# Optimization experiments

Measured on AMD Instinct MI355X. Metric: run time of the kernel, lower is better.

The kernel has to match this reference:

```python
import jax, jax.numpy as jnp
import numpy as np

K = 20  # neighbors

def _graph_feature(x, k):
    # x: (B, N, 3) -> (B, 3, N, k) neighbor features (DGCNN-style gather)
    inner = -2.0 * jnp.einsum('bnd,bmd->bnm', x, x)
    xx = jnp.sum(x * x, axis=2, keepdims=True)              # (B, N, 1)
    pairwise = -xx - inner - jnp.swapaxes(xx, 1, 2)          # (B, N, N) = -||xi-xj||^2
    _, idx = jax.lax.top_k(pairwise, k)                      # (B, N, k) nearest neighbors
    feat = jax.vmap(lambda xb, ib: xb[ib])(x, idx)           # (B, N, k, 3)
    return jnp.transpose(feat, (0, 3, 1, 2))                 # (B, 3, N, k)

def _vn_layer(x, w, scale, shift):
    # matmul over channel dim, folded-BN affine, relu
    y = jnp.einsum('oc,bcnk->bonk', w, x)
    y = y * scale[None, :, None, None] + shift[None, :, None, None]
    return jax.nn.relu(y)

def setup_inputs() -> dict:
    key = jax.random.key(0)
    ks = jax.random.split(key, 12)
    B, N = 32, 256
    inp = {
        'x': jax.random.normal(ks[0], (B, N, 3), dtype=jnp.float32),
        'w1': jax.random.normal(ks[1], (64, 3), dtype=jnp.float32),
        's1': jnp.ones((64,), jnp.float32), 't1': jnp.zeros((64,), jnp.float32),
        'w2': jax.random.normal(ks[2], (128, 64), dtype=jnp.float32) * 0.1,
        's2': jnp.ones((128,), jnp.float32), 't2': jnp.zeros((128,), jnp.float32),
        'w3': jax.random.normal(ks[3], (256, 128), dtype=jnp.float32) * 0.1,
        's3': jnp.ones((256,), jnp.float32), 't3': jnp.zeros((256,), jnp.float32),
        'fc1_w': jax.random.normal(ks[4], (128, 256), dtype=jnp.float32) * 0.05,
        'fc1_b': jnp.zeros((128,), jnp.float32),
        'fc2_w': jax.random.normal(ks[5], (40, 128), dtype=jnp.float32) * 0.05,
        'fc2_b': jnp.zeros((40,), jnp.float32),
    }
    return inp

def reference(x, w1, s1, t1, w2, s2, t2, w3, s3, t3, fc1_w, fc1_b, fc2_w, fc2_b):
    h = _graph_feature(x, K)                                 # (B, 3, N, k)
    h = jax.nn.relu(_vn_layer(h, w1, s1, t1))                # double relu as in source
    h = jax.nn.relu(_vn_layer(h, w2, s2, t2))
    h = jax.nn.relu(_vn_layer(h, w3, s3, t3))                # (B, 256, N, k)
    h = jnp.max(h, axis=-1)                                  # (B, 256, N) with N==256
    h = jax.nn.relu(h @ fc1_w.T + fc1_b)                     # Linear over last axis
    return h @ fc2_w.T + fc2_b                               # (B, 256, 40)
```

## Files before the change

kernel.cpp:

```cpp
#include <hip/hip_runtime.h>
#include <hip/hip_bf16.h>

#define B_ 32
#define N_ 256
#define K_ 20
#define C1 64
#define C2 128
#define C3 256
#define F1 128
#define F2 40
#define NEG_INF (-3.402823466e38f)

__global__ __launch_bounds__(256) void k_front(const float* __restrict__ x,
    const float* __restrict__ w1, const float* __restrict__ s1, const float* __restrict__ b1,
    const float* __restrict__ w2, const float* __restrict__ s2, const float* __restrict__ b2,
    const float* __restrict__ w3, const float* __restrict__ s3, const float* __restrict__ b3,
    const float* __restrict__ fc1w,
    int* __restrict__ idx, float* __restrict__ P, float* __restrict__ fc1T) {

    __shared__ float smem[3136];
    const int blk  = blockIdx.x;
    const int t    = threadIdx.x;
    const int lane = t & 63;
    const int wv   = t >> 6;

    if (blk < 512) {
        float* xs = smem;
        float* y1 = smem + 64;
        float* y2 = smem + 1088;
        const int pbase = blk * 16;
        const int og = t >> 2;
        const int p0 = (t & 3) * 4;

        if (t < 48) xs[t] = x[(size_t)pbase * 3 + t];
        __syncthreads();

        {
            const int oc = lane;
            const float wa = w1[oc * 3 + 0], wb = w1[oc * 3 + 1], wc = w1[oc * 3 + 2];
            const float sc = s1[oc], sh = b1[oc];
            const int q0 = wv * 4;
            float4 v;
            #pragma unroll
            for (int p = 0; p < 4; ++p) {
                const int pp = q0 + p;
                float vv = wa * xs[pp * 3 + 0] + wb * xs[pp * 3 + 1] + wc * xs[pp * 3 + 2];
                (&v.x)[p] = fmaxf(vv * sc + sh, 0.0f);
            }
            *(float4*)&y1[oc * 16 + q0] = v;
        }
        __syncthreads();

        {
            const int oc0 = og * 2;
            float acc[2][4] = {};
            for (int k = 0; k < C1; k += 4) {
                float4 a[4];
                #pragma unroll
                for (int kk = 0; kk < 4; ++kk)
                    a[kk] = *(const float4*)&y1[(k + kk) * 16 + p0];
                const float4 wA = *(const float4*)(w2 + (size_t)oc0 * C1 + k);
                const float4 wB = *(const float4*)(w2 + (size_t)(oc0 + 1) * C1 + k);
                #pragma unroll
                for (int kk = 0; kk < 4; ++kk) {
                    #pragma unroll
                    for (int p = 0; p < 4; ++p) {
                        acc[0][p] += (&wA.x)[kk] * (&a[kk].x)[p];
                        acc[1][p] += (&wB.x)[kk] * (&a[kk].x)[p];
                    }
                }
            }
            const float sc0 = s2[oc0], sh0 = b2[oc0];
            const float sc1 = s2[oc0 + 1], sh1 = b2[oc0 + 1];
            float4 v0, v1;
            #pragma unroll
            for (int p = 0; p < 4; ++p) {
                (&v0.x)[p] = fmaxf(acc[0][p] * sc0 + sh0, 0.0f);
                (&v1.x)[p] = fmaxf(acc[1][p] * sc1 + sh1, 0.0f);
            }
            *(float4*)&y2[oc0 * 16 + p0]       = v0;
            *(float4*)&y2[(oc0 + 1) * 16 + p0] = v1;
        }
        __syncthreads();

        {
            const int oc0 = og * 4;
            float acc[4][4] = {};
            for (int k = 0; k < C2; k += 4) {
                float4 a[4];
                #pragma unroll
                for (int kk = 0; kk < 4; ++kk)
                    a[kk] = *(const float4*)&y2[(k + kk) * 16 + p0];
                float4 w[4];
                #pragma unroll
                for (int o = 0; o < 4; ++o)
                    w[o] = *(const float4*)(w3 + (size_t)(oc0 + o) * C2 + k);
                #pragma unroll
                for (int o = 0; o < 4; ++o) {
                    #pragma unroll
                    for (int kk = 0; kk < 4; ++kk) {
                        const float wvv = (&w[o].x)[kk];
                        #pragma unroll
                        for (int p = 0; p < 4; ++p)
                            acc[o][p] += wvv * (&a[kk].x)[p];
                    }
                }
            }
            const float4 sc = *(const float4*)&s3[oc0];
            const float4 sh = *(const float4*)&b3[oc0];
            #pragma unroll
            for (int p = 0; p < 4; ++p) {
                float4 v;
                #pragma unroll
                for (int o = 0; o < 4; ++o)
                    (&v.x)[o] = fmaxf(acc[o][p] * (&sc.x)[o] + (&sh.x)[o], 0.0f);
                *(float4*)&P[(size_t)(pbase + p0 + p) * C3 + oc0] = v;
            }
        }

    } else if (blk < 2560) {
        const int tb = blk - 512;
        const int b  = tb >> 6;
        const int n  = ((tb & 63) << 2) | wv;
        const int bn = (b << 8) | n;
        const float* xb = x + (size_t)b * N_ * 3;

        const float nx = xb[n * 3 + 0], ny = xb[n * 3 + 1], nz = xb[n * 3 + 2];
        const float xxn = nx * nx + ny * ny + nz * nz;

        unsigned k0, k1, k2, k3;
        {
            unsigned kk[4];
            #pragma unroll
            for (int i = 0; i < 4; ++i) {
                const int m = lane + (i << 6);
                const float cx = xb[m * 3 + 0], cy = xb[m * 3 + 1], cz = xb[m * 3 + 2];
                const float xxm = cx * cx + cy * cy + cz * cz;
                const float v = 2.0f * (nx * cx + ny * cy + nz * cz) - xxn - xxm;
                const unsigned u = __float_as_uint(v);
                kk[i] = (u & 0x80000000u) ? ~u : (u | 0x80000000u);
            }
            k0 = kk[0]; k1 = kk[1]; k2 = kk[2]; k3 = kk[3];
        }

        unsigned prefix = 0u;
        #pragma unroll
        for (int bit = 30; bit >= 0; --bit) {
            const unsigned cand = prefix | (1u << bit);
            const int c = __popcll(__ballot(k0 >= cand))
                        + __popcll(__ballot(k1 >= cand))
                        + __popcll(__ballot(k2 >= cand))
                        + __popcll(__ballot(k3 >= cand));
            if (c >= K_) prefix = cand;
        }
        const unsigned T = prefix;

        int* op = idx + (size_t)bn * K_;
        const unsigned long long lt = (1ull << lane) - 1ull;

        const unsigned long long G0 = __ballot(k0 > T);
        const unsigned long long G1 = __ballot(k1 > T);
        const unsigned long long G2 = __ballot(k2 > T);
        const unsigned long long G3 = __ballot(k3 > T);
        const int n0 = __popcll(G0), n1 = __popcll(G1), n2 = __popcll(G2), n3 = __popcll(G3);
        const int g = n0 + n1 + n2 + n3;
        if (k0 > T) op[          __popcll(G0 & lt)] = lane;
        if (k1 > T) op[n0      + __popcll(G1 & lt)] = 64  | lane;
        if (k2 > T) op[n0 + n1 + __popcll(G2 & lt)] = 128 | lane;
        if (k3 > T) op[n0 + n1 + n2 + __popcll(G3 & lt)] = 192 | lane;

        const int e = K_ - g;
        const unsigned long long E0 = __ballot(k0 == T);
        const unsigned long long E1 = __ballot(k1 == T);
        const unsigned long long E2 = __ballot(k2 == T);
        const unsigned long long E3 = __ballot(k3 == T);
        const int m0 = __popcll(E0), m1 = __popcll(E1), m2 = __popcll(E2);
        if (k0 == T) { const int p = __popcll(E0 & lt);                 if (p < e) op[g + p] = lane; }
        if (k1 == T) { const int p = m0 + __popcll(E1 & lt);            if (p < e) op[g + p] = 64  | lane; }
        if (k2 == T) { const int p = m0 + m1 + __popcll(E2 & lt);       if (p < e) op[g + p] = 128 | lane; }
        if (k3 == T) { const int p = m0 + m1 + m2 + __popcll(E3 & lt);  if (p < e) op[g + p] = 192 | lane; }

    } else {
        const int g = (blk - 2560) * 256 + t;
        #pragma unroll
        for (int i = 0; i < 8; ++i) {
            const int e = g + i * 4096;
            const int j = e >> 8, nn = e & 255;
            fc1T[nn * F1 + j] = fc1w[e];
        }
    }
}

#define GLT_S 20
__global__ __launch_bounds__(256) void k_gfc(const float* __restrict__ P,
                                             const int* __restrict__ idx,
                                             const float* __restrict__ fc1T,
                                             const float* __restrict__ fc1b,
                                             const float* __restrict__ fc2w,
                                             const float* __restrict__ fc2b,
                                             float* __restrict__ out) {
    const int b    = blockIdx.x >> 4;
    const int ch0  = (blockIdx.x & 15) * 16;
    const int t    = threadIdx.x;
    const int lane = t & 63;

    __shared__ float smem[14848];
    float* Ht    = smem;
    float* ftile = smem + 4096;
    float* glT   = smem + 12288;
    float* w2l   = smem;

    {
        const int q  = t & 3;
        const int nl = t >> 2;
        const float* Pq = P + (size_t)b * N_ * C3 + ch0 + q * 4;
        #pragma unroll
        for (int r = 0; r < 4; ++r) {
            const int n = r * 64 + nl;
            const int* ib = idx + ((size_t)((b << 8) | n)) * K_;
            float4 m = make_float4(NEG_INF, NEG_INF, NEG_INF, NEG_INF);
            #pragma unroll
            for (int j = 0; j < K_; ++j) {
                const int id = ib[j];
                const float4 p = *(const float4*)(Pq + (size_t)id * C3);
                m.x = fmaxf(m.x, p.x);
                m.y = fmaxf(m.y, p.y);
                m.z = fmaxf(m.z, p.z);
                m.w = fmaxf(m.w, p.w);
            }
            *(float4*)&Ht[n * 16 + q * 4] = m;
        }
    }
    __syncthreads();

    {
        const int c0 = (t >> 6) * 4;
        float acc[2][4] = {};
        for (int nt = 0; nt < 4; ++nt) {
            {
                const float4* src = (const float4*)(fc1T + (size_t)nt * 64 * F1);
                float4* dst = (float4*)ftile;
                #pragma unroll
                for (int i = 0; i < 8; ++i)
                    dst[t + i * 256] = src[t + i * 256];
            }
            __syncthreads();
            #pragma unroll 4
            for (int nn = 0; nn < 64; ++nn) {
                const int n = nt * 64 + nn;
                const float2 w = *(const float2*)&ftile[nn * F1 + lane * 2];
                const float4 a = *(const float4*)&Ht[n * 16 + c0];
                #pragma unroll
                for (int c = 0; c < 4; ++c) {
                    acc[0][c] += w.x * (&a.x)[c];
                    acc[1][c] += w.y * (&a.x)[c];
                }
            }
            __syncthreads();
        }
        const float bb0 = fc1b[lane * 2], bb1 = fc1b[lane * 2 + 1];
        float4 va, vb;
        #pragma unroll
        for (int c = 0; c < 4; ++c) {
            (&va.x)[c] = fmaxf(acc[0][c] + bb0, 0.0f);
            (&vb.x)[c] = fmaxf(acc[1][c] + bb1, 0.0f);
        }
        *(float4*)&glT[(lane * 2)     * GLT_S + c0] = va;
        *(float4*)&glT[(lane * 2 + 1) * GLT_S + c0] = vb;
    }
    for (int e = t; e < F2 * F1; e += 256)
        w2l[(e >> 7) * 129 + (e & 127)] = fc2w[e];
    __syncthreads();

    {
        const int m   = t & 63;
        const int cig = t >> 6;
        if (m < F2) {
            float a0 = 0.f, a1 = 0.f, a2 = 0.f, a3 = 0.f;
            const float* wr = w2l + m * 129;
            const float* gp = glT + cig * 4;
            #pragma unroll 4
            for (int j = 0; j < F1; ++j) {
                const float w = wr[j];
                const float4 gv = *(const float4*)(gp + j * GLT_S);
                a0 += w * gv.x;
                a1 += w * gv.y;
                a2 += w * gv.z;
                a3 += w * gv.w;
            }
            const float bb = fc2b[m];
            const size_t rb = (size_t)(b * C3 + ch0 + cig * 4) * F2 + m;
            out[rb]          = a0 + bb;
            out[rb + F2]     = a1 + bb;
            out[rb + 2 * F2] = a2 + bb;
            out[rb + 3 * F2] = a3 + bb;
        }
    }
}

extern "C" void kernel_launch(void* const* d_in, const int* in_sizes, int n_in,
                              void* d_out, int out_size, void* d_ws, size_t ws_size,
                              hipStream_t stream) {
    const float* x    = (const float*)d_in[0];
    const float* w1   = (const float*)d_in[1];
    const float* s1   = (const float*)d_in[2];
    const float* t1   = (const float*)d_in[3];
    const float* w2   = (const float*)d_in[4];
    const float* s2   = (const float*)d_in[5];
    const float* t2   = (const float*)d_in[6];
    const float* w3   = (const float*)d_in[7];
    const float* s3   = (const float*)d_in[8];
    const float* t3   = (const float*)d_in[9];
    const float* fc1w = (const float*)d_in[10];
    const float* fc1b = (const float*)d_in[11];
    const float* fc2w = (const float*)d_in[12];
    const float* fc2b = (const float*)d_in[13];
    float* out = (float*)d_out;

    char* ws = (char*)d_ws;
    int*   idx  = (int*)ws;
    float* P    = (float*)(ws + (size_t)B_ * N_ * K_ * 4);
    float* fc1T = P + (size_t)B_ * N_ * C3;

    k_front<<<2576, 256, 0, stream>>>(x, w1, s1, t1, w2, s2, t2, w3, s3, t3,
                                      fc1w, idx, P, fc1T);
    k_gfc<<<B_ * 16, 256, 0, stream>>>(P, idx, fc1T, fc1b, fc2w, fc2b, out);
}
```

Baseline: 123.5 us.

## Compute fc2 from register-held fc1 outputs with DPP row reductions

```diff
diff --git a/kernel.cpp b/kernel.cpp
--- a/kernel.cpp
+++ b/kernel.cpp
@@ -10,6 +10,18 @@
 #define F1 128
 #define F2 40
 #define NEG_INF (-3.402823466e38f)
+
+template <int CTRL>
+__device__ __forceinline__ float dpp_mov(float v) {
+    return __int_as_float(__builtin_amdgcn_update_dpp(0, __float_as_int(v), CTRL, 0xF, 0xF, true));
+}
+__device__ __forceinline__ float row16_sum(float v) {
+    v += dpp_mov<0xB1>(v);
+    v += dpp_mov<0x4E>(v);
+    v += dpp_mov<0x141>(v);
+    v += dpp_mov<0x140>(v);
+    return v;
+}
 
 __global__ __launch_bounds__(256) void k_front(const float* __restrict__ x,
     const float* __restrict__ w1, const float* __restrict__ s1, const float* __restrict__ b1,
@@ -191,7 +203,6 @@
     }
 }
 
-#define GLT_S 20
 __global__ __launch_bounds__(256) void k_gfc(const float* __restrict__ P,
                                              const int* __restrict__ idx,
                                              const float* __restrict__ fc1T,
@@ -203,12 +214,13 @@
     const int ch0  = (blockIdx.x & 15) * 16;
     const int t    = threadIdx.x;
     const int lane = t & 63;
-
-    __shared__ float smem[14848];
+    const int wv   = t >> 6;
+
+    __shared__ float smem[15488];
     float* Ht    = smem;
     float* ftile = smem + 4096;
-    float* glT   = smem + 12288;
-    float* w2l   = smem;
+    float* part  = smem + 12288;
+    float* w2s   = smem;
 
     {
         const int q  = t & 3;
@@ -217,25 +229,30 @@
         #pragma unroll
         for (int r = 0; r < 4; ++r) {
             const int n = r * 64 + nl;
-            const int* ib = idx + ((size_t)((b << 8) | n)) * K_;
+            const int4* ib4 = (const int4*)(idx + ((size_t)((b << 8) | n)) * K_);
             float4 m = make_float4(NEG_INF, NEG_INF, NEG_INF, NEG_INF);
             #pragma unroll
-            for (int j = 0; j < K_; ++j) {
-                const int id = ib[j];
-                const float4 p = *(const float4*)(Pq + (size_t)id * C3);
-                m.x = fmaxf(m.x, p.x);
-                m.y = fmaxf(m.y, p.y);
-                m.z = fmaxf(m.z, p.z);
-                m.w = fmaxf(m.w, p.w);
+            for (int jv = 0; jv < 5; ++jv) {
+                const int4 id4 = ib4[jv];
+                #pragma unroll
+                for (int jj = 0; jj < 4; ++jj) {
+                    const int id = (&id4.x)[jj];
+                    const float4 p = *(const float4*)(Pq + (size_t)id * C3);
+                    m.x = fmaxf(m.x, p.x);
+                    m.y = fmaxf(m.y, p.y);
+                    m.z = fmaxf(m.z, p.z);
+                    m.w = fmaxf(m.w, p.w);
+                }
             }
             *(float4*)&Ht[n * 16 + q * 4] = m;
         }
     }
     __syncthreads();
 
+    const int c0 = wv * 4;
+    float va[4], vb[4];
     {
-        const int c0 = (t >> 6) * 4;
-        float acc[2][4] = {};
+        float acc0[4] = {}, acc1[4] = {};
         for (int nt = 0; nt < 4; ++nt) {
             {
                 const float4* src = (const float4*)(fc1T + (size_t)nt * 64 * F1);
@@ -252,48 +269,59 @@
                 const float4 a = *(const float4*)&Ht[n * 16 + c0];
                 #pragma unroll
                 for (int c = 0; c < 4; ++c) {
-                    acc[0][c] += w.x * (&a.x)[c];
-                    acc[1][c] += w.y * (&a.x)[c];
+                    acc0[c] += w.x * (&a.x)[c];
+                    acc1[c] += w.y * (&a.x)[c];
                 }
             }
             __syncthreads();
         }
         const float bb0 = fc1b[lane * 2], bb1 = fc1b[lane * 2 + 1];
-        float4 va, vb;
         #pragma unroll
         for (int c = 0; c < 4; ++c) {
-            (&va.x)[c] = fmaxf(acc[0][c] + bb0, 0.0f);
-            (&vb.x)[c] = fmaxf(acc[1][c] + bb1, 0.0f);
-        }
-        *(float4*)&glT[(lane * 2)     * GLT_S + c0] = va;
-        *(float4*)&glT[(lane * 2 + 1) * GLT_S + c0] = vb;
-    }
-    for (int e = t; e < F2 * F1; e += 256)
-        w2l[(e >> 7) * 129 + (e & 127)] = fc2w[e];
+            va[c] = fmaxf(acc0[c] + bb0, 0.0f);
+            vb[c] = fmaxf(acc1[c] + bb1, 0.0f);
+        }
+    }
+
+    for (int e = t; e < F2 * 64; e += 256) {
+        const int m = e >> 6, l = e & 63;
+        const int o = m * 134 + 2 * l + 2 * (l >> 4);
+        w2s[o]     = fc2w[m * F1 + 2 * l];
+        w2s[o + 1] = fc2w[m * F1 + 2 * l + 1];
+    }
     __syncthreads();
 
     {
-        const int m   = t & 63;
-        const int cig = t >> 6;
-        if (m < F2) {
-            float a0 = 0.f, a1 = 0.f, a2 = 0.f, a3 = 0.f;
-            const float* wr = w2l + m * 129;
-            const float* gp = glT + cig * 4;
-            #pragma unroll 4
-            for (int j = 0; j < F1; ++j) {
-                const float w = wr[j];
-                const float4 gv = *(const float4*)(gp + j * GLT_S);
-                a0 += w * gv.x;
-                a1 += w * gv.y;
-                a2 += w * gv.z;
-                a3 += w * gv.w;
-            }
-            const float bb = fc2b[m];
-            const size_t rb = (size_t)(b * C3 + ch0 + cig * 4) * F2 + m;
-            out[rb]          = a0 + bb;
-            out[rb + F2]     = a1 + bb;
-            out[rb + 2 * F2] = a2 + bb;
-            out[rb + 3 * F2] = a3 + bb;
+        const int woff = 2 * lane + 2 * (lane >> 4);
+        const int prow = lane >> 4;
+        float* pb = part + wv * 800;
+        const bool writer = (lane & 15) == 0;
+        for (int m = 0; m < F2; ++m) {
+            const float2 wp = *(const float2*)&w2s[m * 134 + woff];
+            float p0 = wp.x * va[0] + wp.y * vb[0];
+            float p1 = wp.x * va[1] + wp.y * vb[1];
+            float p2 = wp.x * va[2] + wp.y * vb[2];
+            float p3 = wp.x * va[3] + wp.y * vb[3];
+            p0 = row16_sum(p0);
+            p1 = row16_sum(p1);
+            p2 = row16_sum(p2);
+            p3 = row16_sum(p3);
+            if (writer) {
+                float4 pv = make_float4(p0, p1, p2, p3);
+                *(float4*)&pb[m * 20 + prow * 4] = pv;
+            }
+        }
+    }
+    __syncthreads();
+
+    {
+        const float* pb = part + wv * 800;
+        const int bch = b * C3 + ch0 + wv * 4;
+        for (int o = lane; o < 160; o += 64) {
+            const int m = o % 40, cc = o / 40;
+            const float* pp = pb + m * 20 + cc;
+            const float v = pp[0] + pp[4] + pp[8] + pp[12] + fc2b[m];
+            out[(size_t)(bch + cc) * F2 + m] = v;
         }
     }
 }
```

Measured after the change: 126.5 us. +2.4%, slower.
